# Kernel optimization log

Hardware: AMD Instinct MI355X
Metric: run time of the kernel (lower is better)

## Reference

```python
import jax, jax.numpy as jnp
import numpy as np

F = 128   # num_features
H = 128   # hidden sizes
U = 128   # u_size == out_size
N = 50000
E = 600000
B = 64
L = 4     # hops + 1 layers


def _scatter_mean(vals, idx, num_segments):
    s = jax.ops.segment_sum(vals, idx, num_segments=num_segments)
    cnt = jax.ops.segment_sum(jnp.ones((vals.shape[0],), vals.dtype), idx,
                              num_segments=num_segments)
    return s / jnp.maximum(cnt, 1.0)[:, None]


def setup_inputs() -> dict:
    key = jax.random.key(0)
    ks = jax.random.split(key, 20)
    x = jax.random.normal(ks[0], (N, F), jnp.float32)
    edge_index = jax.random.randint(ks[1], (2, E), 0, N, jnp.int64)
    u = jax.random.normal(ks[2], (B, U), jnp.float32)
    batch = jnp.sort(jax.random.randint(ks[3], (N,), 0, B, jnp.int64))
    sc = 0.05
    # stacked per-layer params (all layer dims identical since u_size==out_size)
    params = {
        'n1w1': jax.random.normal(ks[4], (L, F, H), jnp.float32) * sc,
        'n1b1': jnp.zeros((L, H), jnp.float32),
        'n1w2': jax.random.normal(ks[5], (L, H, H), jnp.float32) * sc,
        'n1b2': jnp.zeros((L, H), jnp.float32),
        'n2w1': jax.random.normal(ks[6], (L, F + H + U, H), jnp.float32) * sc,
        'n2b1': jnp.zeros((L, H), jnp.float32),
        'n2w2': jax.random.normal(ks[7], (L, H, F), jnp.float32) * sc,
        'n2b2': jnp.zeros((L, F), jnp.float32),
        'gw1': jax.random.normal(ks[8], (L, F + U, H), jnp.float32) * sc,
        'gb1': jnp.zeros((L, H), jnp.float32),
        'gw2': jax.random.normal(ks[9], (L, H, U), jnp.float32) * sc,
        'gb2': jnp.zeros((L, U), jnp.float32),
    }
    return dict(x=x, edge_index=edge_index, u=u, batch=batch, **params)


def reference(x, edge_index, u, batch,
              n1w1, n1b1, n1w2, n1b2, n2w1, n2b1, n2w2, n2b2,
              gw1, gb1, gw2, gb2):
    row, col = edge_index[0], edge_index[1]
    for l in range(L):
        # NodeModel
        m = jax.nn.relu(x[row] @ n1w1[l] + n1b1[l]) @ n1w2[l] + n1b2[l]  # [E,H]
        agg = _scatter_mean(m, col, N)                                    # [N,H]
        h = jnp.concatenate([x, agg, u[batch]], axis=1)                   # [N,F+H+U]
        x = jax.nn.relu(h @ n2w1[l] + n2b1[l]) @ n2w2[l] + n2b2[l]        # [N,F]
        # GlobalModel (uses updated x)
        g = jnp.concatenate([u, _scatter_mean(x, batch, B)], axis=1)      # [B,F+U]
        u = jax.nn.relu(g @ gw1[l] + gb1[l]) @ gw2[l] + gb2[l]            # [B,U]
    return (x, u)
```

## Files before the change

kernel.cpp:

```cpp
#include <hip/hip_runtime.h>

typedef __bf16 bf16;
typedef bf16 bf16x8 __attribute__((ext_vector_type(8)));
typedef bf16 bf16x4 __attribute__((ext_vector_type(4)));
typedef bf16 bf16x2 __attribute__((ext_vector_type(2)));
typedef float floatx4 __attribute__((ext_vector_type(4)));

#define MFMA __builtin_amdgcn_mfma_f32_16x16x32_bf16
#define SCHED_FENCE() __builtin_amdgcn_sched_barrier(0)

__device__ __forceinline__ float bfhi_f(unsigned u) {
  const unsigned x = u << 16;
  return __builtin_bit_cast(float, x);
}
__device__ __forceinline__ float bflo_f(unsigned u) {
  const unsigned x = u & 0xffff0000u;
  return __builtin_bit_cast(float, x);
}

__device__ __forceinline__ void bar_lds() {
  asm volatile("s_waitcnt lgkmcnt(0)" ::: "memory");
  __builtin_amdgcn_s_barrier();
}


__global__ void hist_kernel(const int* __restrict__ ei, int* __restrict__ cnt, int E) {
  int e = blockIdx.x * blockDim.x + threadIdx.x;
  if (e < E) atomicAdd(&cnt[ei[E + e]], 1);
}

__global__ void gcnt_kernel(const int* __restrict__ batch, int* __restrict__ gcnt,
                            int N, int B) {
  const int b = threadIdx.x;
  if (b >= B) return;
  auto lb = [&](int v) {
    int lo = 0, hi = N;
    while (lo < hi) {
      const int mid = (lo + hi) >> 1;
      if (batch[mid] < v) lo = mid + 1; else hi = mid;
    }
    return lo;
  };
  gcnt[b] = lb(b + 1) - lb(b);
}

__global__ void scan1_kernel(const int* __restrict__ cnt, int* __restrict__ colptr,
                             int* __restrict__ rctr, int* __restrict__ btot, int n) {
  __shared__ int sd[256];
  const int tid = threadIdx.x;
  const int i0 = blockIdx.x * 2048 + tid * 8;
  int v[8];
  int tot = 0;
#pragma unroll
  for (int j = 0; j < 8; ++j) {
    const int i = i0 + j;
    v[j] = (i < n) ? cnt[i] : 0;
    tot += v[j];
  }
  sd[tid] = tot;
  __syncthreads();
  for (int off = 1; off < 256; off <<= 1) {
    const int t = (tid >= off) ? sd[tid - off] : 0;
    __syncthreads();
    sd[tid] += t;
    __syncthreads();
  }
  int excl = sd[tid] - tot;
#pragma unroll
  for (int j = 0; j < 8; ++j) {
    const int i = i0 + j;
    if (i < n) { colptr[i] = excl; rctr[i] = excl; }
    excl += v[j];
  }
  if (tid == 255) btot[blockIdx.x] = sd[255];
}

__global__ void scan2_kernel(int* __restrict__ colptr, int* __restrict__ rctr,
                             const int* __restrict__ btot, int n) {
  __shared__ int off_s;
  const int tid = threadIdx.x;
  if (blockIdx.x == 0) return;
  if (tid == 0) {
    int o = 0;
    for (int j = 0; j < (int)blockIdx.x; ++j) o += btot[j];
    off_s = o;
  }
  __syncthreads();
  const int off = off_s;
  const int i0 = blockIdx.x * 2048 + tid * 8;
#pragma unroll
  for (int j = 0; j < 8; ++j) {
    const int i = i0 + j;
    if (i < n) { colptr[i] += off; rctr[i] += off; }
  }
}

__global__ void place_kernel(const int* __restrict__ ei, int* __restrict__ rctr,
                             int* __restrict__ esrow, int E) {
  int e = blockIdx.x * blockDim.x + threadIdx.x;
  if (e >= E) return;
  const int r = ei[e];
  const int c = ei[E + e];
  const int p = atomicAdd(&rctr[c], 1);
  esrow[p] = r;
}

__global__ void wsplit_kernel(const float* __restrict__ src, bf16* __restrict__ dst,
                              int Ksrc, int K, int HH) {
  const int l = blockIdx.y;
  const int gid = blockIdx.x * blockDim.x + threadIdx.x;
  if (gid >= K * HH) return;
  const int h = gid / K, k = gid - h * K;
  const float v = src[(size_t)l * Ksrc * HH + (size_t)k * HH + h];
  const bf16 hi = (bf16)v;
  const bf16 lo = (bf16)(v - (float)hi);
  bf16* d = dst + (size_t)l * 2 * K * HH;
  d[(size_t)h * K + k] = hi;
  d[(size_t)K * HH + (size_t)h * K + k] = lo;
}

__global__ void xsplit_kernel(const float* __restrict__ x, bf16* __restrict__ xhi,
                              bf16* __restrict__ xlo, int n4) {
  const int i = blockIdx.x * 256 + threadIdx.x;
  if (i >= n4) return;
  const float4 v = ((const float4*)x)[i];
  bf16x4 h, l;
  const float vv[4] = {v.x, v.y, v.z, v.w};
#pragma unroll
  for (int r = 0; r < 4; ++r) {
    h[r] = (bf16)vv[r];
    l[r] = (bf16)(vv[r] - (float)h[r]);
  }
  *(bf16x4*)&xhi[(size_t)i * 4] = h;
  *(bf16x4*)&xlo[(size_t)i * 4] = l;
}

__global__ __launch_bounds__(256, 3)
void pnode_mfma(const bf16* __restrict__ xh, const bf16* __restrict__ xl,
                const bf16* __restrict__ w1t, const float* __restrict__ b1,
                const bf16* __restrict__ w2t, const float* __restrict__ b2,
                bf16* __restrict__ P, int N) {
  __shared__ __align__(16) bf16 R[2 * 64 * 136];

  const int tid = threadIdx.x;
  const int n0 = blockIdx.x * 64;
  const int wave = tid >> 6, lane = tid & 63, q = lane >> 4, lr = lane & 15;
  const int hbase = wave * 32;

  int nn[4];
#pragma unroll
  for (int nt = 0; nt < 4; ++nt) {
    int n = n0 + nt * 16 + lr;
    nn[nt] = (n > N - 1) ? (N - 1) : n;
  }

  const floatx4 zz = {0.f, 0.f, 0.f, 0.f};
  floatx4 acc[2][4];
#pragma unroll
  for (int mt = 0; mt < 2; ++mt)
#pragma unroll
    for (int nt = 0; nt < 4; ++nt) acc[mt][nt] = zz;

  {
    bf16x8 bh[2][4], bl[2][4], ah[2][2], al[2][2];
    auto loadA = [&](int kc, int buf) {
#pragma unroll
      for (int mt = 0; mt < 2; ++mt) {
        const bf16* wp = w1t + (size_t)(hbase + mt * 16 + lr) * 128 + kc * 32 + q * 8;
        ah[buf][mt] = *(const bf16x8*)wp;
        al[buf][mt] = *(const bf16x8*)(wp + 16384);
      }
    };
    auto loadB = [&](int kc, int buf) {
#pragma unroll
      for (int nt = 0; nt < 4; ++nt) {
        const size_t off = (size_t)nn[nt] * 128 + kc * 32 + q * 8;
        bh[buf][nt] = *(const bf16x8*)(xh + off);
        bl[buf][nt] = *(const bf16x8*)(xl + off);
      }
    };
    loadA(0, 0);
    loadB(0, 0);
#pragma unroll
    for (int kc = 0; kc < 4; ++kc) {
      const int cur = kc & 1, nxt = cur ^ 1;
      if (kc < 3) {
        loadA(kc + 1, nxt);
        loadB(kc + 1, nxt);
      }
      SCHED_FENCE();
#pragma unroll
      for (int nt = 0; nt < 4; ++nt)
#pragma unroll
        for (int mt = 0; mt < 2; ++mt) {
          acc[mt][nt] = MFMA(ah[cur][mt], bh[cur][nt], acc[mt][nt], 0, 0, 0);
          acc[mt][nt] = MFMA(al[cur][mt], bh[cur][nt], acc[mt][nt], 0, 0, 0);
          acc[mt][nt] = MFMA(ah[cur][mt], bl[cur][nt], acc[mt][nt], 0, 0, 0);
        }
    }
  }

  bf16x8 a2h[2][2], a2l[2][2];
#pragma unroll
  for (int mt = 0; mt < 2; ++mt) {
    const bf16* wp = w2t + (size_t)(hbase + mt * 16 + lr) * 128 + q * 8;
    a2h[0][mt] = *(const bf16x8*)wp;
    a2l[0][mt] = *(const bf16x8*)(wp + 16384);
  }
  SCHED_FENCE();

#pragma unroll
  for (int mt = 0; mt < 2; ++mt) {
    const int h0 = hbase + mt * 16 + q * 4;
    const float* bp = &b1[h0];
#pragma unroll
    for (int nt = 0; nt < 4; ++nt) {
      const int e = nt * 16 + lr;
      bf16x4 hh, ll;
#pragma unroll
      for (int r = 0; r < 4; ++r) {
        const float v = fmaxf(acc[mt][nt][r] + bp[r], 0.f);
        hh[r] = (bf16)v;
        ll[r] = (bf16)(v - (float)hh[r]);
      }
      *(bf16x4*)&R[e * 136 + h0] = hh;
      *(bf16x4*)&R[64 * 136 + e * 136 + h0] = ll;
      acc[mt][nt] = zz;
    }
  }
  bar_lds();

#pragma unroll
  for (int ks = 0; ks < 4; ++ks) {
    const int cur = ks & 1, nxt = cur ^ 1;
    if (ks < 3) {
#pragma unroll
      for (int mt = 0; mt < 2; ++mt) {
        const bf16* wp = w2t + (size_t)(hbase + mt * 16 + lr) * 128 + (ks + 1) * 32 + q * 8;
        a2h[nxt][mt] = *(const bf16x8*)wp;
        a2l[nxt][mt] = *(const bf16x8*)(wp + 16384);
      }
    }
    SCHED_FENCE();
    bf16x8 b2h[4], b2l[4];
#pragma unroll
    for (int nt = 0; nt < 4; ++nt) {
      const bf16* hp = &R[(nt * 16 + lr) * 136 + ks * 32 + q * 8];
      b2h[nt] = *(const bf16x8*)hp;
      b2l[nt] = *(const bf16x8*)(hp + 64 * 136);
    }
#pragma unroll
    for (int nt = 0; nt < 4; ++nt)
#pragma unroll
      for (int mt = 0; mt < 2; ++mt) {
        acc[mt][nt] = MFMA(a2h[cur][mt], b2h[nt], acc[mt][nt], 0, 0, 0);
        acc[mt][nt] = MFMA(a2l[cur][mt], b2h[nt], acc[mt][nt], 0, 0, 0);
        acc[mt][nt] = MFMA(a2h[cur][mt], b2l[nt], acc[mt][nt], 0, 0, 0);
      }
  }
  bar_lds();

#pragma unroll
  for (int mt = 0; mt < 2; ++mt) {
    const int f0 = hbase + mt * 16 + q * 4;
    const float* bp = &b2[f0];
#pragma unroll
    for (int nt = 0; nt < 4; ++nt) {
      const int e = nt * 16 + lr;
      bf16x4 o;
#pragma unroll
      for (int r = 0; r < 4; ++r) o[r] = (bf16)(acc[mt][nt][r] + bp[r]);
      *(bf16x4*)&R[e * 136 + f0] = o;
    }
  }
  bar_lds();
#pragma unroll
  for (int it = 0; it < 4; ++it) {
    const int idx = it * 256 + tid;
    const int row = idx >> 4;
    const int f8 = (idx & 15) * 8;
    const int n = n0 + row;
    if (n < N)
      *(bf16x8*)&P[(size_t)n * 128 + f8] = *(const bf16x8*)&R[row * 136 + f8];
  }
}

__global__ __launch_bounds__(256, 8)
void agg_csr(const bf16* __restrict__ P, const int* __restrict__ colptr,
             const int* __restrict__ esrow,
             bf16* __restrict__ aggh, bf16* __restrict__ aggl, int N, int E) {
  const int lane = threadIdx.x & 63;
  const int c = blockIdx.x * 4 + (threadIdx.x >> 6);
  if (c >= N) return;
  const int beg = colptr[c];
  const int end = (c == N - 1) ? E : colptr[c + 1];
  float s0[4] = {0.f, 0.f, 0.f, 0.f};
  float s1[4] = {0.f, 0.f, 0.f, 0.f};
  int e = beg;
  for (; e + 8 <= end; e += 8) {
    int r[8];
#pragma unroll
    for (int j = 0; j < 8; ++j) r[j] = esrow[e + j];
    unsigned v[8];
#pragma unroll
    for (int j = 0; j < 8; ++j)
      v[j] = *(const unsigned*)&P[(size_t)r[j] * 128 + lane * 2];
#pragma unroll
    for (int j = 0; j < 8; ++j) {
      s0[j & 3] += bfhi_f(v[j]);
      s1[j & 3] += bflo_f(v[j]);
    }
  }
  const int rem = end - e;
  if (rem > 0) {
    int r[8];
#pragma unroll
    for (int j = 0; j < 8; ++j) r[j] = esrow[e + (j < rem ? j : 0)];
    unsigned v[8];
#pragma unroll
    for (int j = 0; j < 8; ++j)
      v[j] = *(const unsigned*)&P[(size_t)r[j] * 128 + lane * 2];
#pragma unroll
    for (int j = 0; j < 8; ++j) {
      if (j < rem) {
        s0[j & 3] += bfhi_f(v[j]);
        s1[j & 3] += bflo_f(v[j]);
      }
    }
  }
  const int cc = end - beg;
  const float inv = 1.f / (float)(cc > 1 ? cc : 1);
  const float v0 = ((s0[0] + s0[1]) + (s0[2] + s0[3])) * inv;
  const float v1 = ((s1[0] + s1[1]) + (s1[2] + s1[3])) * inv;
  bf16x2 h, l;
  h[0] = (bf16)v0;  l[0] = (bf16)(v0 - (float)h[0]);
  h[1] = (bf16)v1;  l[1] = (bf16)(v1 - (float)h[1]);
  *(bf16x2*)&aggh[(size_t)c * 128 + lane * 2] = h;
  *(bf16x2*)&aggl[(size_t)c * 128 + lane * 2] = l;
}

__global__ __launch_bounds__(256, 3)
void node_p(bf16* xh, bf16* xl,
            const bf16* __restrict__ aggh, const bf16* __restrict__ aggl,
            const float* __restrict__ UW, const int* __restrict__ batch,
            const bf16* __restrict__ w1t, const bf16* __restrict__ w2t,
            const float* __restrict__ b2,
            const bf16* __restrict__ w1te, const float* __restrict__ b1e,
            const bf16* __restrict__ w2te, const float* __restrict__ b2e,
            bf16* __restrict__ Pout, float* __restrict__ gx,
            float* __restrict__ xout, int write_x, int has_next, int N) {
  __shared__ __align__(16) bf16 R[2 * 64 * 136];
  __shared__ int sbatch[64];

  const int tid = threadIdx.x;
  const int n0 = blockIdx.x * 64;
  const int wave = tid >> 6, lane = tid & 63, q = lane >> 4, lr = lane & 15;
  const int hbase = wave * 32;

  if (tid < 64) {
    int n = n0 + tid;
    sbatch[tid] = batch[(n > N - 1) ? (N - 1) : n];
  }

  int nn[4], ub[4];
#pragma unroll
  for (int nt = 0; nt < 4; ++nt) {
    int n = n0 + nt * 16 + lr;
    if (n > N - 1) n = N - 1;
    nn[nt] = n;
    ub[nt] = batch[n];
  }

  floatx4 acc[2][4];
#pragma unroll
  for (int mt = 0; mt < 2; ++mt)
#pragma unroll
    for (int nt = 0; nt < 4; ++nt)
      acc[mt][nt] = *(const floatx4*)&UW[(size_t)ub[nt] * 128 + hbase + mt * 16 + q * 4];

  {
    bf16x8 bh[2][4], bl[2][4], ah[2][2], al[2][2];
    auto loadB = [&](int kc, int buf) {
#pragma unroll
      for (int nt = 0; nt < 4; ++nt) {
        if (kc < 4) {
          const size_t off = (size_t)nn[nt] * 128 + kc * 32 + q * 8;
          bh[buf][nt] = *(const bf16x8*)(xh + off);
          bl[buf][nt] = *(const bf16x8*)(xl + off);
        } else {
          const size_t off = (size_t)nn[nt] * 128 + (kc - 4) * 32 + q * 8;
          bh[buf][nt] = *(const bf16x8*)(aggh + off);
          bl[buf][nt] = *(const bf16x8*)(aggl + off);
        }
      }
    };
    auto loadA = [&](int kc, int buf) {
#pragma unroll
      for (int mt = 0; mt < 2; ++mt) {
        const bf16* wp = w1t + (size_t)(hbase + mt * 16 + lr) * 256 + kc * 32 + q * 8;
        ah[buf][mt] = *(const bf16x8*)wp;
        al[buf][mt] = *(const bf16x8*)(wp + 32768);
      }
    };
    loadA(0, 0);
    loadB(0, 0);
#pragma unroll
    for (int kc = 0; kc < 8; ++kc) {
      const int cur = kc & 1, nxt = cur ^ 1;
      if (kc < 7) {
        loadA(kc + 1, nxt);
        loadB(kc + 1, nxt);
      }
      SCHED_FENCE();
#pragma unroll
      for (int nt = 0; nt < 4; ++nt)
#pragma unroll
        for (int mt = 0; mt < 2; ++mt) {
          acc[mt][nt] = MFMA(ah[cur][mt], bh[cur][nt], acc[mt][nt], 0, 0, 0);
          acc[mt][nt] = MFMA(al[cur][mt], bh[cur][nt], acc[mt][nt], 0, 0, 0);
          acc[mt][nt] = MFMA(ah[cur][mt], bl[cur][nt], acc[mt][nt], 0, 0, 0);
        }
    }
  }

  bf16x8 a2h[2][2], a2l[2][2];
#pragma unroll
  for (int mt = 0; mt < 2; ++mt) {
    const bf16* wp = w2t + (size_t)(hbase + mt * 16 + lr) * 128 + q * 8;
    a2h[0][mt] = *(const bf16x8*)wp;
    a2l[0][mt] = *(const bf16x8*)(wp + 16384);
  }
  SCHED_FENCE();

  const floatx4 zz = {0.f, 0.f, 0.f, 0.f};
#pragma unroll
  for (int mt = 0; mt < 2; ++mt) {
    const int h0 = hbase + mt * 16 + q * 4;
#pragma unroll
    for (int nt = 0; nt < 4; ++nt) {
      const int e = nt * 16 + lr;
      bf16x4 hh, ll;
#pragma unroll
      for (int r = 0; r < 4; ++r) {
        const float v = fmaxf(acc[mt][nt][r], 0.f);
        hh[r] = (bf16)v;
        ll[r] = (bf16)(v - (float)hh[r]);
      }
      *(bf16x4*)&R[e * 136 + h0] = hh;
      *(bf16x4*)&R[64 * 136 + e * 136 + h0] = ll;
      acc[mt][nt] = zz;
    }
  }
  bar_lds();

#pragma unroll
  for (int ks = 0; ks < 4; ++ks) {
    const int cur = ks & 1, nxt = cur ^ 1;
    if (ks < 3) {
#pragma unroll
      for (int mt = 0; mt < 2; ++mt) {
        const bf16* wp = w2t + (size_t)(hbase + mt * 16 + lr) * 128 + (ks + 1) * 32 + q * 8;
        a2h[nxt][mt] = *(const bf16x8*)wp;
        a2l[nxt][mt] = *(const bf16x8*)(wp + 16384);
      }
    }
    SCHED_FENCE();
    bf16x8 b2h[4], b2l[4];
#pragma unroll
    for (int nt = 0; nt < 4; ++nt) {
      const bf16* hp = &R[(nt * 16 + lr) * 136 + ks * 32 + q * 8];
      b2h[nt] = *(const bf16x8*)hp;
      b2l[nt] = *(const bf16x8*)(hp + 64 * 136);
    }
#pragma unroll
    for (int nt = 0; nt < 4; ++nt)
#pragma unroll
      for (int mt = 0; mt < 2; ++mt) {
        acc[mt][nt] = MFMA(a2h[cur][mt], b2h[nt], acc[mt][nt], 0, 0, 0);
        acc[mt][nt] = MFMA(a2l[cur][mt], b2h[nt], acc[mt][nt], 0, 0, 0);
        acc[mt][nt] = MFMA(a2h[cur][mt], b2l[nt], acc[mt][nt], 0, 0, 0);
      }
  }
  bar_lds();

  bf16x8 pah[2][2], pal[2][2];
  if (has_next) {
#pragma unroll
    for (int mt = 0; mt < 2; ++mt) {
      const bf16* wp = w1te + (size_t)(hbase + mt * 16 + lr) * 128 + q * 8;
      pah[0][mt] = *(const bf16x8*)wp;
      pal[0][mt] = *(const bf16x8*)(wp + 16384);
    }
    SCHED_FENCE();
  }

  float* Xt = (float*)&R[0];
#pragma unroll
  for (int mt = 0; mt < 2; ++mt) {
    const int f0 = hbase + mt * 16 + q * 4;
    const float* bp = &b2[f0];
#pragma unroll
    for (int nt = 0; nt < 4; ++nt) {
      const int e = nt * 16 + lr;
      const int n = n0 + e;
      float4 o;
      o.x = (n < N) ? acc[mt][nt][0] + bp[0] : 0.f;
      o.y = (n < N) ? acc[mt][nt][1] + bp[1] : 0.f;
      o.z = (n < N) ? acc[mt][nt][2] + bp[2] : 0.f;
      o.w = (n < N) ? acc[mt][nt][3] + bp[3] : 0.f;
      *(float4*)&Xt[e * 132 + f0] = o;
    }
  }
  bar_lds();

  if (has_next) {
#pragma unroll
    for (int it = 0; it < 4; ++it) {
      const int idx = it * 256 + tid;
      const int row = idx >> 4;
      const int f8 = (idx & 15) * 8;
      const int n = n0 + row;
      if (n < N) {
        bf16x8 hh, ll;
#pragma unroll
        for (int j = 0; j < 8; ++j) {
          const float v = Xt[row * 132 + f8 + j];
          hh[j] = (bf16)v;
          ll[j] = (bf16)(v - (float)hh[j]);
        }
        *(bf16x8*)&xh[(size_t)n * 128 + f8] = hh;
        *(bf16x8*)&xl[(size_t)n * 128 + f8] = ll;
      }
    }
  }
  if (write_x) {
#pragma unroll
    for (int it = 0; it < 8; ++it) {
      const int idx = it * 256 + tid;
      const int row = idx >> 5;
      const int f4 = (idx & 31) * 4;
      const int n = n0 + row;
      if (n < N)
        *(float4*)&xout[(size_t)n * 128 + f4] = *(const float4*)&Xt[row * 132 + f4];
    }
  }

  {
    const int f = tid & 127;
    const int es = (tid >> 7) * 32;
    int cur = sbatch[es];
    float s = 0.f;
    for (int e = es; e < es + 32; ++e) {
      const int b = sbatch[e];
      const float v = Xt[e * 132 + f];
      if (b != cur) {
        atomicAdd(&gx[(size_t)cur * 128 + f], s);
        s = 0.f;
        cur = b;
      }
      s += v;
    }
    atomicAdd(&gx[(size_t)cur * 128 + f], s);
  }

  if (!has_next) return;

  floatx4 pacc[2][4];
#pragma unroll
  for (int mt = 0; mt < 2; ++mt)
#pragma unroll
    for (int nt = 0; nt < 4; ++nt) pacc[mt][nt] = zz;

#pragma unroll
  for (int kc = 0; kc < 4; ++kc) {
    const int cur = kc & 1, nxt = cur ^ 1;
    if (kc < 3) {
#pragma unroll
      for (int mt = 0; mt < 2; ++mt) {
        const bf16* wp = w1te + (size_t)(hbase + mt * 16 + lr) * 128 + (kc + 1) * 32 + q * 8;
        pah[nxt][mt] = *(const bf16x8*)wp;
        pal[nxt][mt] = *(const bf16x8*)(wp + 16384);
      }
    }
    SCHED_FENCE();
    bf16x8 bh[4], bl[4];
#pragma unroll
    for (int nt = 0; nt < 4; ++nt) {
      const float* xp = &Xt[(nt * 16 + lr) * 132 + kc * 32 + q * 8];
#pragma unroll
      for (int r = 0; r < 8; ++r) {
        const float v = xp[r];
        bh[nt][r] = (bf16)v;
        bl[nt][r] = (bf16)(v - (float)bh[nt][r]);
      }
    }
#pragma unroll
    for (int nt = 0; nt < 4; ++nt)
#pragma unroll
      for (int mt = 0; mt < 2; ++mt) {
        pacc[mt][nt] = MFMA(pah[cur][mt], bh[nt], pacc[mt][nt], 0, 0, 0);
        pacc[mt][nt] = MFMA(pal[cur][mt], bh[nt], pacc[mt][nt], 0, 0, 0);
        pacc[mt][nt] = MFMA(pah[cur][mt], bl[nt], pacc[mt][nt], 0, 0, 0);
      }
  }

  bf16x8 p2h[2][2], p2l[2][2];
#pragma unroll
  for (int mt = 0; mt < 2; ++mt) {
    const bf16* wp = w2te + (size_t)(hbase + mt * 16 + lr) * 128 + q * 8;
    p2h[0][mt] = *(const bf16x8*)wp;
    p2l[0][mt] = *(const bf16x8*)(wp + 16384);
  }
  SCHED_FENCE();
  bar_lds();

#pragma unroll
  for (int mt = 0; mt < 2; ++mt) {
    const int h0 = hbase + mt * 16 + q * 4;
    const float* bp = &b1e[h0];
#pragma unroll
    for (int nt = 0; nt < 4; ++nt) {
      const int e = nt * 16 + lr;
      bf16x4 hh, ll;
#pragma unroll
      for (int r = 0; r < 4; ++r) {
        const float v = fmaxf(pacc[mt][nt][r] + bp[r], 0.f);
        hh[r] = (bf16)v;
        ll[r] = (bf16)(v - (float)hh[r]);
      }
      *(bf16x4*)&R[e * 136 + h0] = hh;
      *(bf16x4*)&R[64 * 136 + e * 136 + h0] = ll;
      pacc[mt][nt] = zz;
    }
  }
  bar_lds();

#pragma unroll
  for (int ks = 0; ks < 4; ++ks) {
    const int cur = ks & 1, nxt = cur ^ 1;
    if (ks < 3) {
#pragma unroll
      for (int mt = 0; mt < 2; ++mt) {
        const bf16* wp = w2te + (size_t)(hbase + mt * 16 + lr) * 128 + (ks + 1) * 32 + q * 8;
        p2h[nxt][mt] = *(const bf16x8*)wp;
        p2l[nxt][mt] = *(const bf16x8*)(wp + 16384);
      }
    }
    SCHED_FENCE();
    bf16x8 b2h[4], b2l[4];
#pragma unroll
    for (int nt = 0; nt < 4; ++nt) {
      const bf16* hp = &R[(nt * 16 + lr) * 136 + ks * 32 + q * 8];
      b2h[nt] = *(const bf16x8*)hp;
      b2l[nt] = *(const bf16x8*)(hp + 64 * 136);
    }
#pragma unroll
    for (int nt = 0; nt < 4; ++nt)
#pragma unroll
      for (int mt = 0; mt < 2; ++mt) {
        pacc[mt][nt] = MFMA(p2h[cur][mt], b2h[nt], pacc[mt][nt], 0, 0, 0);
        pacc[mt][nt] = MFMA(p2l[cur][mt], b2h[nt], pacc[mt][nt], 0, 0, 0);
        pacc[mt][nt] = MFMA(p2h[cur][mt], b2l[nt], pacc[mt][nt], 0, 0, 0);
      }
  }
  bar_lds();

#pragma unroll
  for (int mt = 0; mt < 2; ++mt) {
    const int f0 = hbase + mt * 16 + q * 4;
    const float* bp = &b2e[f0];
#pragma unroll
    for (int nt = 0; nt < 4; ++nt) {
      const int e = nt * 16 + lr;
      bf16x4 o;
#pragma unroll
      for (int r = 0; r < 4; ++r) o[r] = (bf16)(pacc[mt][nt][r] + bp[r]);
      *(bf16x4*)&R[e * 136 + f0] = o;
    }
  }
  bar_lds();
#pragma unroll
  for (int it = 0; it < 4; ++it) {
    const int idx = it * 256 + tid;
    const int row = idx >> 4;
    const int f8 = (idx & 15) * 8;
    const int n = n0 + row;
    if (n < N)
      *(bf16x8*)&Pout[(size_t)n * 128 + f8] = *(const bf16x8*)&R[row * 136 + f8];
  }
}

__global__ void uw_kernel(const float* __restrict__ u, const float* __restrict__ w1,
                          const float* __restrict__ b1, float* __restrict__ UW) {
  const int b = blockIdx.x, h = threadIdx.x;
  float s = b1[h];
#pragma unroll 8
  for (int k = 0; k < 128; ++k)
    s = fmaf(u[b * 128 + k], w1[(size_t)(256 + k) * 128 + h], s);
  UW[b * 128 + h] = s;
}

__global__ __launch_bounds__(128)
void gmlp_kernel(const float* __restrict__ uin, float* __restrict__ gx,
                 const int* __restrict__ gcnt,
                 const float* __restrict__ gw1, const float* __restrict__ gb1,
                 const float* __restrict__ gw2, const float* __restrict__ gb2,
                 float* __restrict__ uout,
                 const float* __restrict__ w1n_next,
                 const float* __restrict__ b1n_next,
                 float* __restrict__ UW, int has_next) {
  __shared__ float g[256];
  __shared__ float g1[128];
  const int b = blockIdx.x;
  const int t = threadIdx.x;
  const int c = gcnt[b];
  const float inv = 1.f / (float)(c > 1 ? c : 1);
  g[t] = uin[b * 128 + t];
  g[128 + t] = gx[b * 128 + t] * inv;
  gx[b * 128 + t] = 0.f;
  __syncthreads();
  float acc = gb1[t];
#pragma unroll 8
  for (int k = 0; k < 256; ++k) acc = fmaf(g[k], gw1[k * 128 + t], acc);
  g1[t] = fmaxf(acc, 0.f);
  __syncthreads();
  float acc2 = gb2[t];
#pragma unroll 8
  for (int k = 0; k < 128; ++k) acc2 = fmaf(g1[k], gw2[k * 128 + t], acc2);
  uout[b * 128 + t] = acc2;
  if (has_next) {
    __syncthreads();
    g[t] = acc2;
    __syncthreads();
    float s = b1n_next[t];
#pragma unroll 8
    for (int k = 0; k < 128; ++k)
      s = fmaf(g[k], w1n_next[(size_t)(256 + k) * 128 + t], s);
    UW[b * 128 + t] = s;
  }
}

extern "C" void kernel_launch(void* const* d_in, const int* in_sizes, int n_in,
                              void* d_out, int out_size, void* d_ws, size_t ws_size,
                              hipStream_t stream) {
  constexpr int N = 50000, E = 600000, B = 64, F = 128, L = 4;

  const float* x0    = (const float*)d_in[0];
  const int*   ei    = (const int*)  d_in[1];
  const float* u0    = (const float*)d_in[2];
  const int*   batch = (const int*)  d_in[3];
  const float* n1w1  = (const float*)d_in[4];
  const float* n1b1  = (const float*)d_in[5];
  const float* n1w2  = (const float*)d_in[6];
  const float* n1b2  = (const float*)d_in[7];
  const float* n2w1  = (const float*)d_in[8];
  const float* n2b1  = (const float*)d_in[9];
  const float* n2w2  = (const float*)d_in[10];
  const float* n2b2  = (const float*)d_in[11];
  const float* gw1   = (const float*)d_in[12];
  const float* gb1   = (const float*)d_in[13];
  const float* gw2   = (const float*)d_in[14];
  const float* gb2   = (const float*)d_in[15];
  float* out = (float*)d_out;

  char* p = (char*)d_ws;
  auto carve = [&](size_t bytes) -> void* {
    void* q = (void*)p;
    p += (bytes + 255) & ~(size_t)255;
    return q;
  };
  float* ubuf  = (float*)carve((size_t)B * F * 4);
  float* gx    = (float*)carve((size_t)B * F * 4);
  float* UW    = (float*)carve((size_t)B * F * 4);
  int*   cnt   = (int*)carve((size_t)N * 4);
  int*   colptr= (int*)carve((size_t)(N + 1) * 4);
  int*   rctr  = (int*)carve((size_t)N * 4);
  int*   gcnt  = (int*)carve((size_t)B * 4);
  int*   btot  = (int*)carve(32 * 4);
  int*   esrow = (int*)carve((size_t)E * 4);
  bf16*  xhi   = (bf16*)carve((size_t)N * F * 2);
  bf16*  xlo   = (bf16*)carve((size_t)N * F * 2);
  bf16*  P_a   = (bf16*)carve((size_t)N * F * 2);
  bf16*  P_b   = (bf16*)carve((size_t)N * F * 2);
  bf16*  aggh  = (bf16*)carve((size_t)N * F * 2);
  bf16*  aggl  = (bf16*)carve((size_t)N * F * 2);
  bf16*  w1t_e = (bf16*)carve((size_t)L * 2 * 128 * 128 * 2);
  bf16*  w2t_e = (bf16*)carve((size_t)L * 2 * 128 * 128 * 2);
  bf16*  w1t_n = (bf16*)carve((size_t)L * 2 * 256 * 128 * 2);
  bf16*  w2t_n = (bf16*)carve((size_t)L * 2 * 128 * 128 * 2);

  constexpr int SCAN_BLOCKS = (N + 2047) / 2048;

  hipMemsetAsync(cnt, 0, (size_t)N * 4, stream);
  hipMemsetAsync(gx, 0, (size_t)B * F * 4, stream);
  hist_kernel<<<(E + 255) / 256, 256, 0, stream>>>(ei, cnt, E);
  gcnt_kernel<<<1, 64, 0, stream>>>(batch, gcnt, N, B);
  scan1_kernel<<<SCAN_BLOCKS, 256, 0, stream>>>(cnt, colptr, rctr, btot, N);
  scan2_kernel<<<SCAN_BLOCKS, 256, 0, stream>>>(colptr, rctr, btot, N);
  place_kernel<<<(E + 255) / 256, 256, 0, stream>>>(ei, rctr, esrow, E);
  wsplit_kernel<<<dim3(64, L), 256, 0, stream>>>(n1w1, w1t_e, 128, 128, 128);
  wsplit_kernel<<<dim3(64, L), 256, 0, stream>>>(n1w2, w2t_e, 128, 128, 128);
  wsplit_kernel<<<dim3(128, L), 256, 0, stream>>>(n2w1, w1t_n, 384, 256, 128);
  wsplit_kernel<<<dim3(64, L), 256, 0, stream>>>(n2w2, w2t_n, 128, 128, 128);
  xsplit_kernel<<<(N * F / 4 + 255) / 256, 256, 0, stream>>>(x0, xhi, xlo, N * F / 4);
  uw_kernel<<<B, 128, 0, stream>>>(u0, n2w1, n2b1, UW);

  const int NB = (N + 63) / 64;
  pnode_mfma<<<NB, 256, 0, stream>>>(xhi, xlo, w1t_e, n1b1, w2t_e, n1b2, P_a, N);

  for (int l = 0; l < L; ++l) {
    const float* uin  = l ? ubuf : u0;
    float*       uout = (l == L - 1) ? out + (size_t)N * F : ubuf;
    const int    wx   = (l == L - 1) ? 1 : 0;
    const int    hn   = (l < L - 1) ? 1 : 0;
    const bf16*  Pin  = (l & 1) ? P_b : P_a;
    bf16*        Pout = (l & 1) ? P_a : P_b;
    const int    le   = hn ? (l + 1) : l;

    agg_csr<<<(N + 3) / 4, 256, 0, stream>>>(Pin, colptr, esrow, aggh, aggl, N, E);
    node_p<<<NB, 256, 0, stream>>>(
        xhi, xlo, aggh, aggl, UW, batch,
        w1t_n + (size_t)l * 65536, w2t_n + (size_t)l * 32768,
        n2b2 + l * 128,
        w1t_e + (size_t)le * 32768, n1b1 + le * 128,
        w2t_e + (size_t)le * 32768, n1b2 + le * 128,
        Pout, gx, out, wx, hn, N);
    gmlp_kernel<<<B, 128, 0, stream>>>(
        uin, gx, gcnt,
        gw1 + (size_t)l * 256 * 128, gb1 + l * 128,
        gw2 + (size_t)l * 128 * 128, gb2 + l * 128, uout,
        hn ? (n2w1 + (size_t)(l + 1) * 384 * 128) : n2w1,
        hn ? (n2b1 + (l + 1) * 128) : n2b1,
        UW, hn);
  }
}
```

Baseline: 746.8 us.

## Fold edge MLP second layer into node MLP weights via linearity of mean

```diff
diff --git a/kernel.cpp b/kernel.cpp
--- a/kernel.cpp
+++ b/kernel.cpp
@@ -7,7 +7,6 @@
 typedef float floatx4 __attribute__((ext_vector_type(4)));
 
 #define MFMA __builtin_amdgcn_mfma_f32_16x16x32_bf16
-#define SCHED_FENCE() __builtin_amdgcn_sched_barrier(0)
 
 __device__ __forceinline__ float bfhi_f(unsigned u) {
   const unsigned x = u << 16;
@@ -119,6 +118,21 @@
   d[(size_t)K * HH + (size_t)h * K + k] = lo;
 }
 
+__global__ void wfuse_kernel(const float* __restrict__ n2w1,
+                             const float* __restrict__ n1w2,
+                             float* __restrict__ G) {
+  const int l = blockIdx.y, k = blockIdx.x, h = threadIdx.x;
+  const float* w = n2w1 + (size_t)l * 384 * 128;
+  float* g = G + (size_t)l * 256 * 128;
+  g[(size_t)k * 128 + h] = w[(size_t)k * 128 + h];
+  const float* a = n1w2 + (size_t)l * 128 * 128 + (size_t)k * 128;
+  float s = 0.f;
+#pragma unroll 8
+  for (int j = 0; j < 128; ++j)
+    s = fmaf(a[j], w[(size_t)(128 + j) * 128 + h], s);
+  g[(size_t)(128 + k) * 128 + h] = s;
+}
+
 __global__ void xsplit_kernel(const float* __restrict__ x, bf16* __restrict__ xhi,
                               bf16* __restrict__ xlo, int n4) {
   const int i = blockIdx.x * 256 + threadIdx.x;
@@ -138,9 +152,8 @@
 __global__ __launch_bounds__(256, 3)
 void pnode_mfma(const bf16* __restrict__ xh, const bf16* __restrict__ xl,
                 const bf16* __restrict__ w1t, const float* __restrict__ b1,
-                const bf16* __restrict__ w2t, const float* __restrict__ b2,
                 bf16* __restrict__ P, int N) {
-  __shared__ __align__(16) bf16 R[2 * 64 * 136];
+  __shared__ __align__(16) bf16 R[64 * 136];
 
   const int tid = threadIdx.x;
   const int n0 = blockIdx.x * 64;
@@ -188,7 +201,6 @@
         loadA(kc + 1, nxt);
         loadB(kc + 1, nxt);
       }
-      SCHED_FENCE();
 #pragma unroll
       for (int nt = 0; nt < 4; ++nt)
 #pragma unroll
@@ -200,15 +212,6 @@
     }
   }
 
-  bf16x8 a2h[2][2], a2l[2][2];
-#pragma unroll
-  for (int mt = 0; mt < 2; ++mt) {
-    const bf16* wp = w2t + (size_t)(hbase + mt * 16 + lr) * 128 + q * 8;
-    a2h[0][mt] = *(const bf16x8*)wp;
-    a2l[0][mt] = *(const bf16x8*)(wp + 16384);
-  }
-  SCHED_FENCE();
-
 #pragma unroll
   for (int mt = 0; mt < 2; ++mt) {
     const int h0 = hbase + mt * 16 + q * 4;
@@ -216,61 +219,11 @@
 #pragma unroll
     for (int nt = 0; nt < 4; ++nt) {
       const int e = nt * 16 + lr;
-      bf16x4 hh, ll;
-#pragma unroll
-      for (int r = 0; r < 4; ++r) {
-        const float v = fmaxf(acc[mt][nt][r] + bp[r], 0.f);
-        hh[r] = (bf16)v;
-        ll[r] = (bf16)(v - (float)hh[r]);
-      }
+      bf16x4 hh;
+#pragma unroll
+      for (int r = 0; r < 4; ++r)
+        hh[r] = (bf16)fmaxf(acc[mt][nt][r] + bp[r], 0.f);
       *(bf16x4*)&R[e * 136 + h0] = hh;
-      *(bf16x4*)&R[64 * 136 + e * 136 + h0] = ll;
-      acc[mt][nt] = zz;
-    }
-  }
-  bar_lds();
-
-#pragma unroll
-  for (int ks = 0; ks < 4; ++ks) {
-    const int cur = ks & 1, nxt = cur ^ 1;
-    if (ks < 3) {
-#pragma unroll
-      for (int mt = 0; mt < 2; ++mt) {
-        const bf16* wp = w2t + (size_t)(hbase + mt * 16 + lr) * 128 + (ks + 1) * 32 + q * 8;
-        a2h[nxt][mt] = *(const bf16x8*)wp;
-        a2l[nxt][mt] = *(const bf16x8*)(wp + 16384);
-      }
-    }
-    SCHED_FENCE();
-    bf16x8 b2h[4], b2l[4];
-#pragma unroll
-    for (int nt = 0; nt < 4; ++nt) {
-      const bf16* hp = &R[(nt * 16 + lr) * 136 + ks * 32 + q * 8];
-      b2h[nt] = *(const bf16x8*)hp;
-      b2l[nt] = *(const bf16x8*)(hp + 64 * 136);
-    }
-#pragma unroll
-    for (int nt = 0; nt < 4; ++nt)
-#pragma unroll
-      for (int mt = 0; mt < 2; ++mt) {
-        acc[mt][nt] = MFMA(a2h[cur][mt], b2h[nt], acc[mt][nt], 0, 0, 0);
-        acc[mt][nt] = MFMA(a2l[cur][mt], b2h[nt], acc[mt][nt], 0, 0, 0);
-        acc[mt][nt] = MFMA(a2h[cur][mt], b2l[nt], acc[mt][nt], 0, 0, 0);
-      }
-  }
-  bar_lds();
-
-#pragma unroll
-  for (int mt = 0; mt < 2; ++mt) {
-    const int f0 = hbase + mt * 16 + q * 4;
-    const float* bp = &b2[f0];
-#pragma unroll
-    for (int nt = 0; nt < 4; ++nt) {
-      const int e = nt * 16 + lr;
-      bf16x4 o;
-#pragma unroll
-      for (int r = 0; r < 4; ++r) o[r] = (bf16)(acc[mt][nt][r] + bp[r]);
-      *(bf16x4*)&R[e * 136 + f0] = o;
     }
   }
   bar_lds();
@@ -346,7 +299,6 @@
             const bf16* __restrict__ w1t, const bf16* __restrict__ w2t,
             const float* __restrict__ b2,
             const bf16* __restrict__ w1te, const float* __restrict__ b1e,
-            const bf16* __restrict__ w2te, const float* __restrict__ b2e,
             bf16* __restrict__ Pout, float* __restrict__ gx,
             float* __restrict__ xout, int write_x, int has_next, int N) {
   __shared__ __align__(16) bf16 R[2 * 64 * 136];
@@ -411,7 +363,6 @@
         loadA(kc + 1, nxt);
         loadB(kc + 1, nxt);
       }
-      SCHED_FENCE();
 #pragma unroll
       for (int nt = 0; nt < 4; ++nt)
 #pragma unroll
@@ -430,7 +381,6 @@
     a2h[0][mt] = *(const bf16x8*)wp;
     a2l[0][mt] = *(const bf16x8*)(wp + 16384);
   }
-  SCHED_FENCE();
 
   const floatx4 zz = {0.f, 0.f, 0.f, 0.f};
 #pragma unroll
@@ -464,7 +414,6 @@
         a2l[nxt][mt] = *(const bf16x8*)(wp + 16384);
       }
     }
-    SCHED_FENCE();
     bf16x8 b2h[4], b2l[4];
 #pragma unroll
     for (int nt = 0; nt < 4; ++nt) {
@@ -491,7 +440,6 @@
       pah[0][mt] = *(const bf16x8*)wp;
       pal[0][mt] = *(const bf16x8*)(wp + 16384);
     }
-    SCHED_FENCE();
   }
 
   float* Xt = (float*)&R[0];
@@ -582,7 +530,6 @@
         pal[nxt][mt] = *(const bf16x8*)(wp + 16384);
       }
     }
-    SCHED_FENCE();
     bf16x8 bh[4], bl[4];
 #pragma unroll
     for (int nt = 0; nt < 4; ++nt) {
@@ -603,15 +550,6 @@
         pacc[mt][nt] = MFMA(pah[cur][mt], bl[nt], pacc[mt][nt], 0, 0, 0);
       }
   }
-
-  bf16x8 p2h[2][2], p2l[2][2];
-#pragma unroll
-  for (int mt = 0; mt < 2; ++mt) {
-    const bf16* wp = w2te + (size_t)(hbase + mt * 16 + lr) * 128 + q * 8;
-    p2h[0][mt] = *(const bf16x8*)wp;
-    p2l[0][mt] = *(const bf16x8*)(wp + 16384);
-  }
-  SCHED_FENCE();
   bar_lds();
 
 #pragma unroll
@@ -621,61 +559,11 @@
 #pragma unroll
     for (int nt = 0; nt < 4; ++nt) {
       const int e = nt * 16 + lr;
-      bf16x4 hh, ll;
-#pragma unroll
-      for (int r = 0; r < 4; ++r) {
-        const float v = fmaxf(pacc[mt][nt][r] + bp[r], 0.f);
-        hh[r] = (bf16)v;
-        ll[r] = (bf16)(v - (float)hh[r]);
-      }
+      bf16x4 hh;
+#pragma unroll
+      for (int r = 0; r < 4; ++r)
+        hh[r] = (bf16)fmaxf(pacc[mt][nt][r] + bp[r], 0.f);
       *(bf16x4*)&R[e * 136 + h0] = hh;
-      *(bf16x4*)&R[64 * 136 + e * 136 + h0] = ll;
-      pacc[mt][nt] = zz;
-    }
-  }
-  bar_lds();
-
-#pragma unroll
-  for (int ks = 0; ks < 4; ++ks) {
-    const int cur = ks & 1, nxt = cur ^ 1;
-    if (ks < 3) {
-#pragma unroll
-      for (int mt = 0; mt < 2; ++mt) {
-        const bf16* wp = w2te + (size_t)(hbase + mt * 16 + lr) * 128 + (ks + 1) * 32 + q * 8;
-        p2h[nxt][mt] = *(const bf16x8*)wp;
-        p2l[nxt][mt] = *(const bf16x8*)(wp + 16384);
-      }
-    }
-    SCHED_FENCE();
-    bf16x8 b2h[4], b2l[4];
-#pragma unroll
-    for (int nt = 0; nt < 4; ++nt) {
-      const bf16* hp = &R[(nt * 16 + lr) * 136 + ks * 32 + q * 8];
-      b2h[nt] = *(const bf16x8*)hp;
-      b2l[nt] = *(const bf16x8*)(hp + 64 * 136);
-    }
-#pragma unroll
-    for (int nt = 0; nt < 4; ++nt)
-#pragma unroll
-      for (int mt = 0; mt < 2; ++mt) {
-        pacc[mt][nt] = MFMA(p2h[cur][mt], b2h[nt], pacc[mt][nt], 0, 0, 0);
-        pacc[mt][nt] = MFMA(p2l[cur][mt], b2h[nt], pacc[mt][nt], 0, 0, 0);
-        pacc[mt][nt] = MFMA(p2h[cur][mt], b2l[nt], pacc[mt][nt], 0, 0, 0);
-      }
-  }
-  bar_lds();
-
-#pragma unroll
-  for (int mt = 0; mt < 2; ++mt) {
-    const int f0 = hbase + mt * 16 + q * 4;
-    const float* bp = &b2e[f0];
-#pragma unroll
-    for (int nt = 0; nt < 4; ++nt) {
-      const int e = nt * 16 + lr;
-      bf16x4 o;
-#pragma unroll
-      for (int r = 0; r < 4; ++r) o[r] = (bf16)(pacc[mt][nt][r] + bp[r]);
-      *(bf16x4*)&R[e * 136 + f0] = o;
     }
   }
   bar_lds();
@@ -691,12 +579,16 @@
 }
 
 __global__ void uw_kernel(const float* __restrict__ u, const float* __restrict__ w1,
-                          const float* __restrict__ b1, float* __restrict__ UW) {
+                          const float* __restrict__ b1, const float* __restrict__ pb,
+                          float* __restrict__ UW) {
   const int b = blockIdx.x, h = threadIdx.x;
   float s = b1[h];
 #pragma unroll 8
   for (int k = 0; k < 128; ++k)
     s = fmaf(u[b * 128 + k], w1[(size_t)(256 + k) * 128 + h], s);
+#pragma unroll 8
+  for (int k = 0; k < 128; ++k)
+    s = fmaf(pb[k], w1[(size_t)(128 + k) * 128 + h], s);
   UW[b * 128 + h] = s;
 }
 
@@ -708,6 +600,7 @@
                  float* __restrict__ uout,
                  const float* __restrict__ w1n_next,
                  const float* __restrict__ b1n_next,
+                 const float* __restrict__ pb_next,
                  float* __restrict__ UW, int has_next) {
   __shared__ float g[256];
   __shared__ float g1[128];
@@ -736,6 +629,9 @@
 #pragma unroll 8
     for (int k = 0; k < 128; ++k)
       s = fmaf(g[k], w1n_next[(size_t)(256 + k) * 128 + t], s);
+#pragma unroll 8
+    for (int k = 0; k < 128; ++k)
+      s = fmaf(pb_next[k], w1n_next[(size_t)(128 + k) * 128 + t], s);
     UW[b * 128 + t] = s;
   }
 }
@@ -785,9 +681,9 @@
   bf16*  aggh  = (bf16*)carve((size_t)N * F * 2);
   bf16*  aggl  = (bf16*)carve((size_t)N * F * 2);
   bf16*  w1t_e = (bf16*)carve((size_t)L * 2 * 128 * 128 * 2);
-  bf16*  w2t_e = (bf16*)carve((size_t)L * 2 * 128 * 128 * 2);
   bf16*  w1t_n = (bf16*)carve((size_t)L * 2 * 256 * 128 * 2);
   bf16*  w2t_n = (bf16*)carve((size_t)L * 2 * 128 * 128 * 2);
+  float* wtmp  = (float*)carve((size_t)L * 256 * 128 * 4);
 
   constexpr int SCAN_BLOCKS = (N + 2047) / 2048;
 
@@ -799,14 +695,14 @@
   scan2_kernel<<<SCAN_BLOCKS, 256, 0, stream>>>(colptr, rctr, btot, N);
   place_kernel<<<(E + 255) / 256, 256, 0, stream>>>(ei, rctr, esrow, E);
   wsplit_kernel<<<dim3(64, L), 256, 0, stream>>>(n1w1, w1t_e, 128, 128, 128);
-  wsplit_kernel<<<dim3(64, L), 256, 0, stream>>>(n1w2, w2t_e, 128, 128, 128);
-  wsplit_kernel<<<dim3(128, L), 256, 0, stream>>>(n2w1, w1t_n, 384, 256, 128);
+  wfuse_kernel<<<dim3(128, L), 128, 0, stream>>>(n2w1, n1w2, wtmp);
+  wsplit_kernel<<<dim3(128, L), 256, 0, stream>>>(wtmp, w1t_n, 256, 256, 128);
   wsplit_kernel<<<dim3(64, L), 256, 0, stream>>>(n2w2, w2t_n, 128, 128, 128);
   xsplit_kernel<<<(N * F / 4 + 255) / 256, 256, 0, stream>>>(x0, xhi, xlo, N * F / 4);
-  uw_kernel<<<B, 128, 0, stream>>>(u0, n2w1, n2b1, UW);
+  uw_kernel<<<B, 128, 0, stream>>>(u0, n2w1, n2b1, n1b2, UW);
 
   const int NB = (N + 63) / 64;
-  pnode_mfma<<<NB, 256, 0, stream>>>(xhi, xlo, w1t_e, n1b1, w2t_e, n1b2, P_a, N);
+  pnode_mfma<<<NB, 256, 0, stream>>>(xhi, xlo, w1t_e, n1b1, P_a, N);
 
   for (int l = 0; l < L; ++l) {
     const float* uin  = l ? ubuf : u0;
@@ -823,7 +719,6 @@
         w1t_n + (size_t)l * 65536, w2t_n + (size_t)l * 32768,
         n2b2 + l * 128,
         w1t_e + (size_t)le * 32768, n1b1 + le * 128,
-        w2t_e + (size_t)le * 32768, n1b2 + le * 128,
         Pout, gx, out, wx, hn, N);
     gmlp_kernel<<<B, 128, 0, stream>>>(
         uin, gx, gcnt,
@@ -831,6 +726,7 @@
         gw2 + (size_t)l * 128 * 128, gb2 + l * 128, uout,
         hn ? (n2w1 + (size_t)(l + 1) * 384 * 128) : n2w1,
         hn ? (n2b1 + (l + 1) * 128) : n2b1,
+        hn ? (n1b2 + (l + 1) * 128) : n1b2,
         UW, hn);
   }
 }
```

Result: faster. 695.7 us (-6.8%).
